# Kernel optimization log

Measured on AMD Instinct MI355X. Metric: run time of the kernel, lower is better.

The kernel has to match this reference:

```python
import jax, jax.numpy as jnp
import numpy as np

ROUNDS = 10  # DATA_ROUNDS_PER_GAME


def _lstm_run(x, h0, c0, Wih, Whh, bih, bhh):
    """PyTorch-semantics multi-layer LSTM. x: [B,T,H]; h0,c0: [L,B,H]."""
    L = Wih.shape[0]
    def step(carry, xt):
        h, c = carry
        inp = xt
        hs, cs = [], []
        for l in range(L):
            gates = inp @ Wih[l].T + bih[l] + h[l] @ Whh[l].T + bhh[l]
            i, f, g, o = jnp.split(gates, 4, axis=-1)  # torch gate order i,f,g,o
            cn = jax.nn.sigmoid(f) * c[l] + jax.nn.sigmoid(i) * jnp.tanh(g)
            hn = jax.nn.sigmoid(o) * jnp.tanh(cn)
            hs.append(hn); cs.append(cn)
            inp = hn
        return (jnp.stack(hs), jnp.stack(cs)), inp
    (hT, cT), ys = jax.lax.scan(step, (h0, c0), jnp.swapaxes(x, 0, 1))
    return jnp.swapaxes(ys, 0, 1), hT, cT


def setup_inputs():
    key = jax.random.key(0)
    B, IN, H, L, OUT = 1024, 512, 128, 2, 2
    ks = jax.random.split(key, 16)
    def lin(k, o, i):
        s = 1.0 / np.sqrt(i)
        kw, kb = jax.random.split(k)
        return (jax.random.uniform(kw, (o, i), jnp.float32, -s, s),
                jax.random.uniform(kb, (o,), jnp.float32, -s, s))
    W_in1, b_in1 = lin(ks[0], 2 * IN, IN)
    W_in2, b_in2 = lin(ks[1], H, 2 * IN)
    Wq, bq = lin(ks[2], H, H)
    Wk, bk = lin(ks[3], H, H)
    Wo1, bo1 = lin(ks[4], H // 2, H)
    Wo2, bo2 = lin(ks[5], OUT, H // 2)
    s = 1.0 / np.sqrt(H)
    Wih = jax.random.uniform(ks[6], (L, 4 * H, H), jnp.float32, -s, s)
    Whh = jax.random.uniform(ks[7], (L, 4 * H, H), jnp.float32, -s, s)
    bih = jax.random.uniform(ks[8], (L, 4 * H), jnp.float32, -s, s)
    bhh = jax.random.uniform(ks[9], (L, 4 * H), jnp.float32, -s, s)
    input_vec = jax.random.normal(ks[10], (B, ROUNDS, IN), jnp.float32)
    game_vector = jax.random.normal(ks[11], (B, L, H), jnp.float32) * 0.1
    user_vector = jax.random.normal(ks[12], (B, L, H), jnp.float32) * 0.1
    return dict(input_vec=input_vec, game_vector=game_vector, user_vector=user_vector,
                W_in1=W_in1, b_in1=b_in1, W_in2=W_in2, b_in2=b_in2,
                Wq=Wq, bq=bq, Wk=Wk, bk=bk,
                Wih=Wih, Whh=Whh, bih=bih, bhh=bhh,
                Wo1=Wo1, bo1=bo1, Wo2=Wo2, bo2=bo2)


def reference(input_vec, game_vector, user_vector, W_in1, b_in1, W_in2, b_in2,
              Wq, bq, Wk, bk, Wih, Whh, bih, bhh, Wo1, bo1, Wo2, bo2):
    H = Wq.shape[0]
    shape = user_vector.shape  # (B, L, H)
    # input_fc (Dropout is identity in eval / p=0): Linear->ReLU->Linear->ReLU
    lstm_in = jax.nn.relu(jax.nn.relu(input_vec @ W_in1.T + b_in1) @ W_in2.T + b_in2)
    new_shape = tuple(shape[:-1][::-1]) + (shape[-1],)  # (L, B, H) via reshape, as in torch source
    h = game_vector.reshape(new_shape)
    c = user_vector.reshape(new_shape)
    scale = 1.0 / jnp.sqrt(jnp.float32(H))
    results, attn_list = [], []
    for r in range(ROUNDS):
        rel = lstm_in[:, :r + 1, :]
        hid = []
        for hist in range(r + 1):
            seq = rel[:, hist:, :] if hist > 1 else rel  # faithful to original '> 1' condition
            ys, h, c = _lstm_run(seq, h, c, Wih, Whh, bih, bhh)  # state carries across all runs
            hid.append(ys[:, -1, :])
        M = jnp.stack(hid, axis=1)  # [B, r+1, H]
        Q = M[:, -1:, :] @ Wq.T + bq
        K = M @ Wk.T + bk
        scores = jax.nn.softmax(jnp.einsum('bqh,bkh->bqk', Q, K) * scale, axis=-1)
        V = jax.nn.log_softmax(jax.nn.relu(M @ Wo1.T + bo1) @ Wo2.T + bo2, axis=-1)
        results.append(jnp.einsum('bqk,bkd->bqd', scores, V))
        pad = ROUNDS - (r + 1)
        if pad > 0:
            scores = jnp.pad(scores, ((0, 0), (0, 0), (0, pad)), constant_values=-1.0)
        attn_list.append(scores)
    output = jnp.concatenate(results, axis=1)            # [B, ROUNDS, output_dim]
    attention = jnp.concatenate(attn_list, axis=1)       # [B, ROUNDS, ROUNDS]
    return output, attention, h.reshape(shape), c.reshape(shape)
```

## Files before the change

### kernel.cpp

```cpp
#include <hip/hip_runtime.h>
#include <stdint.h>

static const size_t OFF_ATT = 20480;
static const size_t OFF_H   = 122880;
static const size_t OFF_C   = 385024;

typedef _Float16 f16;
typedef f16 f16x8 __attribute__((ext_vector_type(8)));
typedef float f32x4 __attribute__((ext_vector_type(4)));

__device__ __forceinline__ float sigf(float x) { return 1.0f / (1.0f + __expf(-x)); }
__device__ __forceinline__ float tanhfast(float x) { return 1.0f - 2.0f / (__expf(2.0f * x) + 1.0f); }

#define MFMA16(a, b, c) __builtin_amdgcn_mfma_f32_16x16x32_f16((a), (b), (c), 0, 0, 0)

__global__ void bias_comb_k(const float* __restrict__ bih, const float* __restrict__ bhh,
                            float* __restrict__ b0, float* __restrict__ b1) {
    int i = blockIdx.x * 256 + threadIdx.x;
    if (i < 512) {
        b0[i] = bih[i] + bhh[i];
        b1[i] = bih[512 + i] + bhh[512 + i];
    }
}

__global__ __launch_bounds__(256) void pack_frag_k(const float* __restrict__ W, f16* __restrict__ out,
                                                   int N, int K) {
    int idx = blockIdx.x * 256 + threadIdx.x;
    if (idx >= N * K) return;
    int i = idx & 7, l = (idx >> 3) & 63, rest = idx >> 9;
    int KT = K >> 5;
    int kt = rest % KT, nt = rest / KT;
    int n = nt * 16 + (l & 15);
    int k = kt * 32 + (l >> 4) * 8 + i;
    out[idx] = (f16)W[n * K + k];
}

__global__ __launch_bounds__(256) void reshape_xg_k(const float* __restrict__ xg0, float* __restrict__ xgr) {
    int idx = blockIdx.x * 256 + threadIdx.x;
    int row16 = idx & 15;
    int col   = (idx >> 4) & 511;
    int tb    = idx >> 13;
    int t     = tb % 10, blk = tb / 10;
    xgr[idx] = xg0[(((size_t)(blk * 16 + row16) * 10 + t) << 9) + col];
}

__global__ __launch_bounds__(256) void gemm_bias_act_k(const float* __restrict__ A, const float* __restrict__ Bm,
                                                       const float* __restrict__ bias, float* __restrict__ C,
                                                       int M, int N, int K, int relu) {
    __shared__ float As[16][68];
    __shared__ float Bs[16][68];
    int tid = threadIdx.x;
    int tx = tid & 15, ty = tid >> 4;
    int bm = blockIdx.y << 6, bn = blockIdx.x << 6;
    int lr = tid >> 2, lk = (tid & 3) << 2;
    float acc[4][4] = {};
    for (int k0 = 0; k0 < K; k0 += 16) {
        __syncthreads();
        float4 av = *(const float4*)(A + (size_t)(bm + lr) * K + k0 + lk);
        float4 bv = *(const float4*)(Bm + (size_t)(bn + lr) * K + k0 + lk);
        As[lk + 0][lr] = av.x; As[lk + 1][lr] = av.y; As[lk + 2][lr] = av.z; As[lk + 3][lr] = av.w;
        Bs[lk + 0][lr] = bv.x; Bs[lk + 1][lr] = bv.y; Bs[lk + 2][lr] = bv.z; Bs[lk + 3][lr] = bv.w;
        __syncthreads();
#pragma unroll
        for (int kk = 0; kk < 16; ++kk) {
            float a[4], b[4];
#pragma unroll
            for (int i = 0; i < 4; ++i) a[i] = As[kk][ty * 4 + i];
#pragma unroll
            for (int j = 0; j < 4; ++j) b[j] = Bs[kk][tx * 4 + j];
#pragma unroll
            for (int i = 0; i < 4; ++i)
#pragma unroll
                for (int j = 0; j < 4; ++j) acc[i][j] = fmaf(a[i], b[j], acc[i][j]);
        }
    }
#pragma unroll
    for (int i = 0; i < 4; ++i)
#pragma unroll
        for (int j = 0; j < 4; ++j) {
            float v = acc[i][j] + bias[bn + tx * 4 + j];
            if (relu) v = fmaxf(v, 0.0f);
            C[(size_t)(bm + ty * 4 + i) * N + bn + tx * 4 + j] = v;
        }
}

__global__ __launch_bounds__(512) void recurrent_mfma7_k(
    const float* __restrict__ xgr,
    const f16* __restrict__ Wf,
    const float* __restrict__ bias1,
    const f16* __restrict__ Wqf, const float* __restrict__ bq,
    const f16* __restrict__ Wkf, const float* __restrict__ bk,
    const f16* __restrict__ Wo1f, const float* __restrict__ bo1,
    const float* __restrict__ Wo2, const float* __restrict__ bo2,
    const float* __restrict__ gv, const float* __restrict__ uv,
    float* __restrict__ out) {
    __shared__ __align__(16) f16 hA0[2][2048];
    __shared__ __align__(16) f16 hA1[2][2048];
    __shared__ __align__(16) f16 Ksh[10][16 * 136];
    __shared__ float vsh[10][16][2];
    __shared__ __align__(16) float qsm[16 * 132];
    __shared__ __align__(16) float us[16 * 68];
    __shared__ float scs[16][10];
    __shared__ float wo2s[130];
    __shared__ unsigned long long wbase_s;

    const int tid  = threadIdx.x;
    const int lane = tid & 63;
    const int w    = tid >> 6;
    const int ml   = lane & 15;
    const int qh   = lane >> 4;
    const int blk  = blockIdx.x;
    const int b0   = blk << 4;

    if (tid < 128) wo2s[tid] = Wo2[tid];
    if (tid < 2)   wo2s[128 + tid] = bo2[tid];
    if (tid == 0)  wbase_s = (unsigned long long)(uintptr_t)Wf;

    float bs1v[4];
#pragma unroll
    for (int g = 0; g < 4; ++g) bs1v[g] = bias1[g * 128 + w * 16 + ml];

    const int fo = w * 2048 + lane * 8;

    float c0v[4], c1v[4];
#pragma unroll
    for (int r4 = 0; r4 < 4; ++r4) {
        int row = qh * 4 + r4;
        int b = b0 + row, hj = w * 16 + ml;
        c0v[r4] = uv[(size_t)b * 128 + hj];
        c1v[r4] = uv[131072 + (size_t)b * 128 + hj];
        int ke = hj ^ ((row & 7) << 3);
        hA0[0][row * 128 + ke] = (f16)gv[(size_t)b * 128 + hj];
        hA1[0][row * 128 + ke] = (f16)gv[131072 + (size_t)b * 128 + hj];
    }
    int p = 0;
    __syncthreads();

    auto readA = [&](const f16* base, int kt) -> f16x8 {
        int e = ml * 128 + (((kt << 5) + (qh << 3)) ^ ((ml & 7) << 3));
        return *(const f16x8*)(base + e);
    };

    auto lstm_step = [&](int t) {
        const f16* wf = (const f16*)(uintptr_t)wbase_s;
        f32x4 C0, C1, C2, C3;
        {
            const float* xb = xgr + ((((size_t)blk * 10 + t) << 9) << 4);
            int coff = w * 16 + ml;
            C0 = *(const f32x4*)(xb + ((coff      ) << 4) + qh * 4);
            C1 = *(const f32x4*)(xb + ((coff + 128) << 4) + qh * 4);
            C2 = *(const f32x4*)(xb + ((coff + 256) << 4) + qh * 4);
            C3 = *(const f32x4*)(xb + ((coff + 384) << 4) + qh * 4);
        }
        f16x8 F0[4][4];
#pragma unroll
        for (int kt = 0; kt < 4; ++kt)
#pragma unroll
            for (int g = 0; g < 4; ++g)
                F0[kt][g] = *(const f16x8*)(wf + fo + g * 16384 + kt * 512);
        const f16* h0p = &hA0[p][0];
#pragma unroll
        for (int kt = 0; kt < 4; ++kt) {
            f16x8 a = readA(h0p, kt);
            C0 = MFMA16(a, F0[kt][0], C0);
            C1 = MFMA16(a, F0[kt][1], C1);
            C2 = MFMA16(a, F0[kt][2], C2);
            C3 = MFMA16(a, F0[kt][3], C3);
        }
        f16x8 F1[4][4];
#pragma unroll
        for (int kt = 0; kt < 4; ++kt)
#pragma unroll
            for (int g = 0; g < 4; ++g)
                F1[kt][g] = *(const f16x8*)(wf + 65536 + fo + g * 16384 + kt * 512);
        f16* h0n = &hA0[p ^ 1][0];
#pragma unroll
        for (int r4 = 0; r4 < 4; ++r4) {
            float cn = sigf(C1[r4]) * c0v[r4] + sigf(C0[r4]) * tanhfast(C2[r4]);
            float hn = sigf(C3[r4]) * tanhfast(cn);
            c0v[r4] = cn;
            int row = qh * 4 + r4;
            h0n[row * 128 + ((w * 16 + ml) ^ ((row & 7) << 3))] = (f16)hn;
        }
        __syncthreads();
        C0 = f32x4{bs1v[0], bs1v[0], bs1v[0], bs1v[0]};
        C1 = f32x4{bs1v[1], bs1v[1], bs1v[1], bs1v[1]};
        C2 = f32x4{bs1v[2], bs1v[2], bs1v[2], bs1v[2]};
        C3 = f32x4{bs1v[3], bs1v[3], bs1v[3], bs1v[3]};
#pragma unroll
        for (int kt = 0; kt < 4; ++kt) {
            f16x8 a = readA(h0n, kt);
            C0 = MFMA16(a, F1[kt][0], C0);
            C1 = MFMA16(a, F1[kt][1], C1);
            C2 = MFMA16(a, F1[kt][2], C2);
            C3 = MFMA16(a, F1[kt][3], C3);
        }
        f16x8 F2[4][4];
#pragma unroll
        for (int kt = 0; kt < 4; ++kt)
#pragma unroll
            for (int g = 0; g < 4; ++g)
                F2[kt][g] = *(const f16x8*)(wf + 131072 + fo + g * 16384 + kt * 512);
        const f16* h1p = &hA1[p][0];
#pragma unroll
        for (int kt = 0; kt < 4; ++kt) {
            f16x8 a = readA(h1p, kt);
            C0 = MFMA16(a, F2[kt][0], C0);
            C1 = MFMA16(a, F2[kt][1], C1);
            C2 = MFMA16(a, F2[kt][2], C2);
            C3 = MFMA16(a, F2[kt][3], C3);
        }
        f16* h1n = &hA1[p ^ 1][0];
#pragma unroll
        for (int r4 = 0; r4 < 4; ++r4) {
            float cn = sigf(C1[r4]) * c1v[r4] + sigf(C0[r4]) * tanhfast(C2[r4]);
            float hn = sigf(C3[r4]) * tanhfast(cn);
            c1v[r4] = cn;
            int row = qh * 4 + r4;
            h1n[row * 128 + ((w * 16 + ml) ^ ((row & 7) << 3))] = (f16)hn;
        }
        p ^= 1;
    };

    for (int r = 0; r < 10; ++r) {
        for (int hist = 0; hist <= r; ++hist) {
            const int t0 = (hist <= 1) ? 0 : hist;
            for (int t = t0; t <= r; ++t) lstm_step(t);

            f16x8 Bk[4], Bo[4], Bq[4];
#pragma unroll
            for (int kt = 0; kt < 4; ++kt) Bk[kt] = *(const f16x8*)(Wkf + (((w * 4 + kt) * 64 + lane) << 3));
            if (w < 4) {
#pragma unroll
                for (int kt = 0; kt < 4; ++kt) Bo[kt] = *(const f16x8*)(Wo1f + (((w * 4 + kt) * 64 + lane) << 3));
            }
            if (hist == r) {
#pragma unroll
                for (int kt = 0; kt < 4; ++kt) Bq[kt] = *(const f16x8*)(Wqf + (((w * 4 + kt) * 64 + lane) << 3));
            }
            const float bkv  = bk[w * 16 + ml];
            const float bo1v = (w < 4) ? bo1[w * 16 + ml] : 0.0f;
            __syncthreads();
            const f16* h1c = &hA1[p][0];
            {
                f32x4 C = f32x4{bkv, bkv, bkv, bkv};
#pragma unroll
                for (int kt = 0; kt < 4; ++kt) C = MFMA16(readA(h1c, kt), Bk[kt], C);
#pragma unroll
                for (int r4 = 0; r4 < 4; ++r4) Ksh[hist][(qh * 4 + r4) * 136 + w * 16 + ml] = (f16)C[r4];
            }
            if (w < 4) {
                f32x4 C = f32x4{bo1v, bo1v, bo1v, bo1v};
#pragma unroll
                for (int kt = 0; kt < 4; ++kt) C = MFMA16(readA(h1c, kt), Bo[kt], C);
#pragma unroll
                for (int r4 = 0; r4 < 4; ++r4) us[(qh * 4 + r4) * 68 + w * 16 + ml] = fmaxf(C[r4], 0.f);
            }
            if (hist == r) {
                const float bqv = bq[w * 16 + ml];
                f32x4 C = f32x4{bqv, bqv, bqv, bqv};
#pragma unroll
                for (int kt = 0; kt < 4; ++kt) C = MFMA16(readA(h1c, kt), Bq[kt], C);
#pragma unroll
                for (int r4 = 0; r4 < 4; ++r4) qsm[(qh * 4 + r4) * 132 + w * 16 + ml] = C[r4];
            }
            __syncthreads();
            if (tid < 16) {
                float v0 = wo2s[128], v1 = wo2s[129];
                const float* up = us + tid * 68;
#pragma unroll 8
                for (int k = 0; k < 64; ++k) {
                    float uu = up[k];
                    v0 = fmaf(uu, wo2s[k], v0);
                    v1 = fmaf(uu, wo2s[64 + k], v1);
                }
                float mv = fmaxf(v0, v1);
                float lse = mv + __logf(__expf(v0 - mv) + __expf(v1 - mv));
                vsh[hist][tid][0] = v0 - lse;
                vsh[hist][tid][1] = v1 - lse;
            }
            if (hist == r && tid < 16 * (r + 1)) {
                int row = tid & 15, kk = tid >> 4;
                const float* qp = qsm + row * 132;
                const f16* kp = &Ksh[kk][row * 136];
                float pacc = 0.f;
                for (int k = 0; k < 128; ++k) pacc += qp[k] * (float)kp[k];
                scs[row][kk] = pacc * 0.088388347648318447f;
            }
        }
        __syncthreads();
        if (tid < 16) {
            float mx = -3.4e38f;
            for (int kk = 0; kk <= r; ++kk) mx = fmaxf(mx, scs[tid][kk]);
            float sum = 0.f;
            for (int kk = 0; kk <= r; ++kk) sum += __expf(scs[tid][kk] - mx);
            float inv = 1.0f / sum;
            float o0 = 0.f, o1 = 0.f;
            for (int kk = 0; kk <= r; ++kk) {
                float pp = __expf(scs[tid][kk] - mx) * inv;
                scs[tid][kk] = pp;
                o0 = fmaf(pp, vsh[kk][tid][0], o0);
                o1 = fmaf(pp, vsh[kk][tid][1], o1);
            }
            out[(size_t)(b0 + tid) * 20 + r * 2 + 0] = o0;
            out[(size_t)(b0 + tid) * 20 + r * 2 + 1] = o1;
        }
        __syncthreads();
        if (tid < 160) {
            int row = tid / 10, jp = tid - row * 10;
            out[OFF_ATT + (size_t)(b0 + row) * 100 + (size_t)r * 10 + jp] = (jp <= r) ? scs[row][jp] : -1.0f;
        }
    }

#pragma unroll
    for (int r4 = 0; r4 < 4; ++r4) {
        int row = qh * 4 + r4;
        int b = b0 + row, hj = w * 16 + ml;
        int ke = row * 128 + (hj ^ ((row & 7) << 3));
        out[OFF_H + (size_t)b * 128 + hj]          = (float)hA0[p][ke];
        out[OFF_H + 131072 + (size_t)b * 128 + hj] = (float)hA1[p][ke];
        out[OFF_C + (size_t)b * 128 + hj]          = c0v[r4];
        out[OFF_C + 131072 + (size_t)b * 128 + hj] = c1v[r4];
    }
}

extern "C" void kernel_launch(void* const* d_in, const int* in_sizes, int n_in,
                              void* d_out, int out_size, void* d_ws, size_t ws_size,
                              hipStream_t stream) {
    const float* input_vec = (const float*)d_in[0];
    const float* gv    = (const float*)d_in[1];
    const float* uv    = (const float*)d_in[2];
    const float* W_in1 = (const float*)d_in[3];
    const float* b_in1 = (const float*)d_in[4];
    const float* W_in2 = (const float*)d_in[5];
    const float* b_in2 = (const float*)d_in[6];
    const float* Wq    = (const float*)d_in[7];
    const float* bq    = (const float*)d_in[8];
    const float* Wk    = (const float*)d_in[9];
    const float* bk    = (const float*)d_in[10];
    const float* Wih   = (const float*)d_in[11];
    const float* Whh   = (const float*)d_in[12];
    const float* bih   = (const float*)d_in[13];
    const float* bhh   = (const float*)d_in[14];
    const float* Wo1   = (const float*)d_in[15];
    const float* bo1   = (const float*)d_in[16];
    const float* Wo2   = (const float*)d_in[17];
    const float* bo2   = (const float*)d_in[18];
    float* out = (float*)d_out;
    float* ws  = (float*)d_ws;

    float* tmp1    = ws + 0;
    float* xg0     = ws + 0;
    float* xgr     = ws + 5242880;
    float* lstm_in = ws + 10485760;
    f16*   Wf      = (f16*)(ws + 11796480);
    f16*   Wqf     = (f16*)(ws + 11894784);
    f16*   Wkf     = (f16*)(ws + 11902976);
    f16*   Wo1f    = (f16*)(ws + 11911168);
    float* bias1c  = ws + 11915264;
    float* bias0c  = ws + 11915776;

    pack_frag_k<<<256, 256, 0, stream>>>(Whh,          Wf,           512, 128);
    pack_frag_k<<<256, 256, 0, stream>>>(Wih + 65536,  Wf + 65536,   512, 128);
    pack_frag_k<<<256, 256, 0, stream>>>(Whh + 65536,  Wf + 131072,  512, 128);
    pack_frag_k<<<64,  256, 0, stream>>>(Wq,  Wqf,  128, 128);
    pack_frag_k<<<64,  256, 0, stream>>>(Wk,  Wkf,  128, 128);
    pack_frag_k<<<32,  256, 0, stream>>>(Wo1, Wo1f, 64,  128);
    bias_comb_k<<<2, 256, 0, stream>>>(bih, bhh, bias0c, bias1c);

    gemm_bias_act_k<<<dim3(16, 160), 256, 0, stream>>>(input_vec, W_in1, b_in1, tmp1, 10240, 1024, 512, 1);
    gemm_bias_act_k<<<dim3(2, 160), 256, 0, stream>>>(tmp1, W_in2, b_in2, lstm_in, 10240, 128, 1024, 1);
    gemm_bias_act_k<<<dim3(8, 160), 256, 0, stream>>>(lstm_in, Wih, bias0c, xg0, 10240, 512, 128, 0);
    reshape_xg_k<<<20480, 256, 0, stream>>>(xg0, xgr);

    recurrent_mfma7_k<<<64, 512, 0, stream>>>(xgr, Wf, bias1c,
                                              Wqf, bq, Wkf, bk, Wo1f, bo1, Wo2, bo2,
                                              gv, uv, out);
}
```

Before: 1.375 ms.

## Stage layer-0 recurrent weights in LDS and spill K cache to global

Copies the 128 KB packed layer-0 Whh fragment into shared memory once per block, so the recurrent step reads these weights from LDS instead of reloading them from global or L2 every timestep. To free LDS for this, the per-history K cache moves from shared memory to a global workspace buffer that aliases the now-dead xg0 region, and the score dot product is vectorised to 8-wide f16 loads. The cost is very high LDS use (one block per CU) and extra global traffic and latency for K reads, which depend on the writes from earlier steps being visible after __syncthreads.

```diff
diff --git a/kernel.cpp b/kernel.cpp
--- a/kernel.cpp
+++ b/kernel.cpp
@@ -8,6 +8,7 @@
 typedef _Float16 f16;
 typedef f16 f16x8 __attribute__((ext_vector_type(8)));
 typedef float f32x4 __attribute__((ext_vector_type(4)));
+typedef int i32x4 __attribute__((ext_vector_type(4)));
 
 __device__ __forceinline__ float sigf(float x) { return 1.0f / (1.0f + __expf(-x)); }
 __device__ __forceinline__ float tanhfast(float x) { return 1.0f - 2.0f / (__expf(2.0f * x) + 1.0f); }
@@ -84,7 +85,7 @@
         }
 }
 
-__global__ __launch_bounds__(512) void recurrent_mfma7_k(
+__global__ __launch_bounds__(512) void recurrent_mfma8_k(
     const float* __restrict__ xgr,
     const f16* __restrict__ Wf,
     const float* __restrict__ bias1,
@@ -93,10 +94,11 @@
     const f16* __restrict__ Wo1f, const float* __restrict__ bo1,
     const float* __restrict__ Wo2, const float* __restrict__ bo2,
     const float* __restrict__ gv, const float* __restrict__ uv,
+    f16* __restrict__ Kg,
     float* __restrict__ out) {
+    __shared__ __align__(16) f16 W0s[65536];
     __shared__ __align__(16) f16 hA0[2][2048];
     __shared__ __align__(16) f16 hA1[2][2048];
-    __shared__ __align__(16) f16 Ksh[10][16 * 136];
     __shared__ float vsh[10][16][2];
     __shared__ __align__(16) float qsm[16 * 132];
     __shared__ __align__(16) float us[16 * 68];
@@ -115,6 +117,13 @@
     if (tid < 128) wo2s[tid] = Wo2[tid];
     if (tid < 2)   wo2s[128 + tid] = bo2[tid];
     if (tid == 0)  wbase_s = (unsigned long long)(uintptr_t)Wf;
+
+    {
+        const i32x4* src = (const i32x4*)Wf;
+        i32x4* dst = (i32x4*)W0s;
+#pragma unroll
+        for (int i = 0; i < 16; ++i) dst[tid + i * 512] = src[tid + i * 512];
+    }
 
     float bs1v[4];
 #pragma unroll
@@ -152,20 +161,14 @@
             C2 = *(const f32x4*)(xb + ((coff + 256) << 4) + qh * 4);
             C3 = *(const f32x4*)(xb + ((coff + 384) << 4) + qh * 4);
         }
-        f16x8 F0[4][4];
-#pragma unroll
-        for (int kt = 0; kt < 4; ++kt)
-#pragma unroll
-            for (int g = 0; g < 4; ++g)
-                F0[kt][g] = *(const f16x8*)(wf + fo + g * 16384 + kt * 512);
         const f16* h0p = &hA0[p][0];
 #pragma unroll
         for (int kt = 0; kt < 4; ++kt) {
             f16x8 a = readA(h0p, kt);
-            C0 = MFMA16(a, F0[kt][0], C0);
-            C1 = MFMA16(a, F0[kt][1], C1);
-            C2 = MFMA16(a, F0[kt][2], C2);
-            C3 = MFMA16(a, F0[kt][3], C3);
+            C0 = MFMA16(a, *(const f16x8*)(W0s + fo + 0 * 16384 + kt * 512), C0);
+            C1 = MFMA16(a, *(const f16x8*)(W0s + fo + 1 * 16384 + kt * 512), C1);
+            C2 = MFMA16(a, *(const f16x8*)(W0s + fo + 2 * 16384 + kt * 512), C2);
+            C3 = MFMA16(a, *(const f16x8*)(W0s + fo + 3 * 16384 + kt * 512), C3);
         }
         f16x8 F1[4][4];
 #pragma unroll
@@ -247,7 +250,8 @@
 #pragma unroll
                 for (int kt = 0; kt < 4; ++kt) C = MFMA16(readA(h1c, kt), Bk[kt], C);
 #pragma unroll
-                for (int r4 = 0; r4 < 4; ++r4) Ksh[hist][(qh * 4 + r4) * 136 + w * 16 + ml] = (f16)C[r4];
+                for (int r4 = 0; r4 < 4; ++r4)
+                    Kg[(((size_t)(blk * 10 + hist) * 16 + qh * 4 + r4) << 7) + w * 16 + ml] = (f16)C[r4];
             }
             if (w < 4) {
                 f32x4 C = f32x4{bo1v, bo1v, bo1v, bo1v};
@@ -282,9 +286,14 @@
             if (hist == r && tid < 16 * (r + 1)) {
                 int row = tid & 15, kk = tid >> 4;
                 const float* qp = qsm + row * 132;
-                const f16* kp = &Ksh[kk][row * 136];
+                const f16* kp = Kg + (((size_t)(blk * 10 + kk) * 16 + row) << 7);
                 float pacc = 0.f;
-                for (int k = 0; k < 128; ++k) pacc += qp[k] * (float)kp[k];
+#pragma unroll
+                for (int k8 = 0; k8 < 16; ++k8) {
+                    f16x8 kv = *(const f16x8*)(kp + k8 * 8);
+#pragma unroll
+                    for (int j = 0; j < 8; ++j) pacc += qp[k8 * 8 + j] * (float)kv[j];
+                }
                 scs[row][kk] = pacc * 0.088388347648318447f;
             }
         }
@@ -351,6 +360,7 @@
 
     float* tmp1    = ws + 0;
     float* xg0     = ws + 0;
+    f16*   Kg      = (f16*)ws;
     float* xgr     = ws + 5242880;
     float* lstm_in = ws + 10485760;
     f16*   Wf      = (f16*)(ws + 11796480);
@@ -373,7 +383,7 @@
     gemm_bias_act_k<<<dim3(8, 160), 256, 0, stream>>>(lstm_in, Wih, bias0c, xg0, 10240, 512, 128, 0);
     reshape_xg_k<<<20480, 256, 0, stream>>>(xg0, xgr);
 
-    recurrent_mfma7_k<<<64, 512, 0, stream>>>(xgr, Wf, bias1c,
+    recurrent_mfma8_k<<<64, 512, 0, stream>>>(xgr, Wf, bias1c,
                                               Wqf, bq, Wkf, bk, Wo1f, bo1, Wo2, bo2,
-                                              gv, uv, out);
-}
+                                              gv, uv, Kg, out);
+}
```

Result: slower. 1.456 ms (+5.9%).
